# Kernel tuning notes

Measured on AMD Instinct MI355X. Metric: run time of the kernel, lower is better.

The kernel has to match this reference:

```python
import jax, jax.numpy as jnp
import numpy as np

H, DD, NCLS, NELEM, NPROP = 256, 32, 8, 11, 14
B, N = 4, 4096
ENC = NELEM + NPROP  # 25

_DIMS = [("dc1", ENC, H), ("dc21", H, DD), ("dc22", H, DD),
         ("in1", ENC, H), ("in2", H, H), ("in3", H, H),
         ("conv", H, H),
         ("id1", H, H), ("id2", H, H), ("id3", H, H),
         ("oid", H, NCLS), ("och", H, 2),
         ("m1", H + NCLS, H + NCLS), ("m2", H + NCLS, H), ("m3", H, H), ("om", H, 3)]


def setup_inputs() -> dict:
    key = jax.random.key(0)
    ks = jax.random.split(key, 2 + len(_DIMS))
    X = jax.random.normal(ks[0], (B, N, 15), jnp.float32)
    ids = jax.random.randint(ks[1], (B, N), 0, NELEM).astype(jnp.float32)
    X = X.at[:, :, 0].set(ids)
    d = {"X": X}
    for i, (name, di, do) in enumerate(_DIMS):
        W = jax.random.normal(ks[2 + i], (di, do), jnp.float32) / np.sqrt(di)
        d["W_" + name] = W
        d["b_" + name] = jnp.zeros((do,), jnp.float32)
    return d


def reference(X, W_dc1, b_dc1, W_dc21, b_dc21, W_dc22, b_dc22,
              W_in1, b_in1, W_in2, b_in2, W_in3, b_in3,
              W_conv, b_conv,
              W_id1, b_id1, W_id2, b_id2, W_id3, b_id3,
              W_oid, b_oid, W_och, b_och,
              W_m1, b_m1, W_m2, b_m2, W_m3, b_m3, W_om, b_om):
    act = jax.nn.selu
    # input encoding: one-hot element id (stop-grad via int cast) + properties, then selu
    onehot = jax.nn.one_hot(X[:, :, 0].astype(jnp.int32), NELEM, dtype=X.dtype)
    enc = act(jnp.concatenate([onehot, X[:, :, 1:]], axis=-1))  # [B,N,25]
    # distance coordinates
    h = act(enc @ W_dc1 + b_dc1)
    c1 = h @ W_dc21 + b_dc21  # [B,N,DD]
    c2 = h @ W_dc22 + b_dc22
    # pairwise distance -> exp adjacency
    na = jnp.sum(c1 * c1, -1)[:, :, None]
    nb = jnp.sum(c2 * c2, -1)[:, None, :]
    Dsq = jnp.clip(na - 2.0 * jnp.einsum('bnd,bmd->bnm', c1, c2) + nb, 1e-12, 1e12)
    adj = jnp.exp(-jnp.sqrt(Dsq))  # [B,N,N]
    # node MLP
    x = act(enc @ W_in1 + b_in1)
    x = act(x @ W_in2 + b_in2)
    x = act(x @ W_in3 + b_in3)
    # GraphConv: adj^k @ (x W) + b, k=4 (in-degree norm computed but unused upstream)
    x = act(jnp.einsum('bnm,bmh->bnh', adj ** 4, x @ W_conv) + b_conv)
    # id head
    a = act(x @ W_id1 + b_id1)
    a = act(a @ W_id2 + b_id2)
    a = act(a @ W_id3 + b_id3)
    out_id_logits = a @ W_oid + b_oid  # [B,N,8]
    out_charge = a @ W_och + b_och     # [B,N,2]
    # momentum head
    xb = jnp.concatenate([x, act(out_id_logits)], axis=-1)
    bb = act(xb @ W_m1 + b_m1)
    bb = act(bb @ W_m2 + b_m2)
    bb = act(bb @ W_m3 + b_m3)
    corr = bb @ W_om + b_om  # [B,N,3]
    mom = jnp.stack([X[:, :, 2] + corr[:, :, 0],
                     X[:, :, 3] + corr[:, :, 1],
                     X[:, :, 4] + corr[:, :, 2]], axis=-1)
    return jnp.concatenate([out_id_logits, mom, out_charge], axis=-1)  # [B,N,13]
```

## Files before the change

### kernel.cpp

```cpp
#include <hip/hip_runtime.h>
#include <cstddef>
#include <cstdint>

#define MROWS 16384
#define NSEQ  4096
#define ASTR  296
#define SELU_SCALE  1.0507009873554805f
#define SELU_ASCALE 1.7580993408473766f

typedef short bf16x8 __attribute__((ext_vector_type(8)));
typedef float f32x4  __attribute__((ext_vector_type(4)));

__device__ __forceinline__ float selu_f(float x) {
    return x > 0.f ? SELU_SCALE * x : SELU_ASCALE * (__expf(x) - 1.f);
}
__device__ __forceinline__ unsigned short f2bf(float x) {
    union { float f; unsigned int u; } v; v.f = x;
    unsigned int r = v.u + 0x7fffu + ((v.u >> 16) & 1u);
    return (unsigned short)(r >> 16);
}
__device__ __forceinline__ unsigned short t2bf(float x) {
    union { float f; unsigned int u; } v; v.f = x;
    return (unsigned short)(v.u >> 16);
}

struct PrepEnt { const float* W; unsigned short* WT; int N, K, Nfill, ldw, tileOff, tilesK; };
struct PrepArgs {
    PrepEnt e[16];
    const float *b21, *b22, *boid, *boch, *bdc1, *bin1;
    float *bc12, *boo, *bcat;
};
__global__ __launch_bounds__(256) void prep_kernel(PrepArgs pa) {
    if (blockIdx.y == 1) {
        if (blockIdx.x == 0) {
            int t = threadIdx.x;
            if (t < 32) pa.bc12[t] = pa.b21[t];
            else if (t < 64) pa.bc12[t] = pa.b22[t - 32];
            else if (t < 128) {
                int j = t - 64;
                pa.boo[j] = j < 8 ? pa.boid[j] : (j < 10 ? pa.boch[j - 8] : 0.f);
            }
        } else if (blockIdx.x == 1) {
            pa.bcat[threadIdx.x] = pa.bdc1[threadIdx.x];
        } else if (blockIdx.x == 2) {
            pa.bcat[256 + threadIdx.x] = pa.bin1[threadIdx.x];
        }
        return;
    }
    int bx = blockIdx.x;
    int ei = 0;
#pragma unroll
    for (int e = 1; e < 16; ++e)
        if (bx >= pa.e[e].tileOff) ei = e;
    PrepEnt E = pa.e[ei];
    int local = bx - E.tileOff;
    int tn = local / E.tilesK, tk = local - tn * E.tilesK;
    int k0 = tk * 32, n0 = tn * 32;

    __shared__ float ts[32][33];
    int t = threadIdx.x;
    int kl = t >> 3, nl4 = (t & 7) * 4;
    {
        int gk = k0 + kl;
#pragma unroll
        for (int j = 0; j < 4; ++j) {
            int gn = n0 + nl4 + j;
            float v = (gk < E.K && gn < E.N) ? E.W[(size_t)gk * E.N + gn] : 0.f;
            ts[nl4 + j][kl] = v;
        }
    }
    __syncthreads();
    int nl = t >> 3, kl4 = (t & 7) * 4;
    if (n0 + nl < E.Nfill) {
        ushort4 o;
        o.x = f2bf(ts[nl][kl4 + 0]);
        o.y = f2bf(ts[nl][kl4 + 1]);
        o.z = f2bf(ts[nl][kl4 + 2]);
        o.w = f2bf(ts[nl][kl4 + 3]);
        *(ushort4*)(E.WT + (size_t)(n0 + nl) * E.ldw + k0 + kl4) = o;
    }
}

template <int MT, int NT>
__device__ __forceinline__ void zero_acc(f32x4 (&acc)[MT][NT]) {
#pragma unroll
    for (int i = 0; i < MT; ++i)
#pragma unroll
        for (int nt = 0; nt < NT; ++nt) acc[i][nt] = (f32x4){0.f, 0.f, 0.f, 0.f};
}

template <int MT, int NT, int K>
__device__ __forceinline__ void compute_tiles(
    f32x4 (&acc)[MT][NT],
    const unsigned short* __restrict__ src, int sstr,
    const unsigned short* __restrict__ WT, int ldw,
    int col0, int ln)
{
    int quad = ln >> 4, l15 = ln & 15;
    const unsigned short* wbase = WT + (size_t)(col0 + l15) * ldw + quad * 8;
    bf16x8 bcur[NT];
#pragma unroll
    for (int nt = 0; nt < NT; ++nt)
        bcur[nt] = *(const bf16x8*)(wbase + nt * 16 * ldw);
#pragma unroll
    for (int k0 = 0; k0 < K; k0 += 32) {
        bf16x8 bnxt[NT];
        if (k0 + 32 < K) {
#pragma unroll
            for (int nt = 0; nt < NT; ++nt)
                bnxt[nt] = *(const bf16x8*)(wbase + nt * 16 * ldw + k0 + 32);
        }
#pragma unroll
        for (int i = 0; i < MT; ++i) {
            bf16x8 af = *(const bf16x8*)(src + (i * 16 + l15) * sstr + k0 + quad * 8);
#pragma unroll
            for (int nt = 0; nt < NT; ++nt)
                acc[i][nt] = __builtin_amdgcn_mfma_f32_16x16x32_bf16(af, bcur[nt], acc[i][nt], 0, 0, 0);
        }
        if (k0 + 32 < K) {
#pragma unroll
            for (int nt = 0; nt < NT; ++nt) bcur[nt] = bnxt[nt];
        }
    }
}

template <int MT, int NT>
__device__ __forceinline__ void store_tiles(
    f32x4 (&acc)[MT][NT], unsigned short* __restrict__ dst,
    int col0, const float* __restrict__ bias, int Nreal, int act, int ln)
{
    int quad = ln >> 4, l15 = ln & 15;
#pragma unroll
    for (int nt = 0; nt < NT; ++nt) {
        int col = col0 + nt * 16 + l15;
        float bv = (bias && col < Nreal) ? bias[col] : 0.f;
#pragma unroll
        for (int i = 0; i < MT; ++i) {
#pragma unroll
            for (int r = 0; r < 4; ++r) {
                int row = i * 16 + quad * 4 + r;
                float v = acc[i][nt][r] + bv;
                if (act) v = selu_f(v);
                if (col >= Nreal) v = 0.f;
                dst[row * ASTR + col] = f2bf(v);
            }
        }
    }
}

__global__ __launch_bounds__(512) void pre_mega(
    const float* __restrict__ X,
    const unsigned short* __restrict__ WTd, const float* __restrict__ bcat,
    const unsigned short* __restrict__ WTc12, const float* __restrict__ bc12,
    const unsigned short* __restrict__ WTin2, const float* __restrict__ b_in2,
    const unsigned short* __restrict__ WTin3, const float* __restrict__ b_in3,
    const unsigned short* __restrict__ WTconv,
    unsigned short* __restrict__ c1b, unsigned short* __restrict__ c2b,
    float* __restrict__ n1, float* __restrict__ n2,
    unsigned short* __restrict__ xwTb)
{
    __shared__ unsigned short encs[64 * 32];
    __shared__ unsigned short bufA[64 * ASTR];
    __shared__ unsigned short bufB[64 * ASTR];
    __shared__ float c12s[64 * 68];

    int tid = threadIdx.x, wv = tid >> 6, ln = tid & 63;
    int quad = ln >> 4, l15 = ln & 15;
    int row0 = blockIdx.x * 64;

#pragma unroll
    for (int p = 0; p < 4; ++p) {
        int idx = p * 512 + tid;
        int row = idx >> 5, col = idx & 31;
        float v = 0.f;
        if (col < 11) {
            int id = (int)X[(size_t)(row0 + row) * 15];
            v = (id == col) ? SELU_SCALE : 0.f;
        } else if (col < 25) {
            v = selu_f(X[(size_t)(row0 + row) * 15 + 1 + (col - 11)]);
        }
        encs[row * 32 + col] = f2bf(v);
    }
    __syncthreads();

#pragma unroll
    for (int ph = 0; ph < 2; ++ph) {
        f32x4 acc[4][2]; zero_acc<4, 2>(acc);
        compute_tiles<4, 2, 32>(acc, encs, 32, WTd + (size_t)ph * 256 * 32, 32, wv * 32, ln);
        store_tiles<4, 2>(acc, ph ? bufB : bufA, wv * 32, bcat + ph * 256, 256, 1, ln);
    }
    __syncthreads();

    if (wv < 2) {
        f32x4 acc[4][2]; zero_acc<4, 2>(acc);
        compute_tiles<4, 2, 256>(acc, bufA, ASTR, WTc12, 256, wv * 32, ln);
#pragma unroll
        for (int nt = 0; nt < 2; ++nt) {
            int col = wv * 32 + nt * 16 + l15;
            float bv = bc12[col];
#pragma unroll
            for (int i = 0; i < 4; ++i)
#pragma unroll
                for (int r = 0; r < 4; ++r)
                    c12s[(i * 16 + quad * 4 + r) * 68 + col] = acc[i][nt][r] + bv;
        }
    }
    __syncthreads();

    if (tid < 64) {
        int grow = row0 + tid;
        const float* p = &c12s[tid * 68];
        float s1 = 0.f, s2 = 0.f;
        unsigned int o1[16], o2[16];
#pragma unroll
        for (int k = 0; k < 32; k += 2) {
            float a0 = p[k], a1 = p[k + 1];
            s1 += a0 * a0 + a1 * a1;
            o1[k >> 1] = (unsigned)f2bf(a0) | ((unsigned)f2bf(a1) << 16);
            float b0 = p[32 + k], b1 = p[33 + k];
            s2 += b0 * b0 + b1 * b1;
            o2[k >> 1] = (unsigned)f2bf(b0) | ((unsigned)f2bf(b1) << 16);
        }
        uint4* d1 = (uint4*)(c1b + (size_t)grow * 32);
        uint4* d2 = (uint4*)(c2b + (size_t)grow * 32);
#pragma unroll
        for (int j = 0; j < 4; ++j) {
            d1[j] = make_uint4(o1[4 * j], o1[4 * j + 1], o1[4 * j + 2], o1[4 * j + 3]);
            d2[j] = make_uint4(o2[4 * j], o2[4 * j + 1], o2[4 * j + 2], o2[4 * j + 3]);
        }
        n1[grow] = s1;
        n2[grow] = s2;
    }

    {
        f32x4 acc[4][2]; zero_acc<4, 2>(acc);
        compute_tiles<4, 2, 256>(acc, bufB, ASTR, WTin2, 256, wv * 32, ln);
        store_tiles<4, 2>(acc, bufA, wv * 32, b_in2, 256, 1, ln);
    }
    __syncthreads();
    {
        f32x4 acc[4][2]; zero_acc<4, 2>(acc);
        compute_tiles<4, 2, 256>(acc, bufA, ASTR, WTin3, 256, wv * 32, ln);
        store_tiles<4, 2>(acc, bufB, wv * 32, b_in3, 256, 1, ln);
    }
    __syncthreads();
    {
        f32x4 acc[4][2]; zero_acc<4, 2>(acc);
        compute_tiles<4, 2, 256>(acc, bufB, ASTR, WTconv, 256, wv * 32, ln);
        store_tiles<4, 2>(acc, bufA, wv * 32, nullptr, 256, 0, ln);
    }
    __syncthreads();

    int b = row0 >> 12;
    int c0 = (row0 & 4095) >> 5;
#pragma unroll
    for (int p = 0; p < 4; ++p) {
        int idx = p * 512 + tid;
        int h = idx >> 3, mg = idx & 7;
        unsigned int w[4];
#pragma unroll
        for (int j = 0; j < 4; ++j) {
            unsigned int lo = bufA[(mg * 8 + 2 * j) * ASTR + h];
            unsigned int hi = bufA[(mg * 8 + 2 * j + 1) * ASTR + h];
            w[j] = lo | (hi << 16);
        }
        *(uint4*)(xwTb + ((size_t)((b * 128 + c0 + (mg >> 2)) * 256 + h) * 32) + (mg & 3) * 8) =
            make_uint4(w[0], w[1], w[2], w[3]);
    }
}

__global__ __launch_bounds__(512, 4) void adj_conv_mfma(
    const unsigned short* __restrict__ c1b, const unsigned short* __restrict__ c2b,
    const float* __restrict__ n1, const float* __restrict__ n2,
    const unsigned short* __restrict__ xwTb, const float* __restrict__ bconv,
    unsigned short* __restrict__ xc)
{
    __shared__ unsigned short wls[2][32][72];

    int tid = threadIdx.x, wv = tid >> 6, ln = tid & 63, quad = ln >> 4, l15 = ln & 15;
    int blk = blockIdx.x;
    int b = (blk >> 1) & 3;
    int iidx = ((blk >> 3) << 1) | (blk & 1);
    int i0 = iidx * 32;
    size_t base = (size_t)b * NSEQ;

    int it = wv & 1;
    int mt = wv >> 1;

    bf16x8 c1f = *(const bf16x8*)(c1b + (base + i0 + it * 16 + l15) * 32 + quad * 8);
    float4 n1v = *(const float4*)(n1 + base + i0 + it * 16 + quad * 4);
    const unsigned short* xwb = xwTb + (size_t)b * 128 * 256 * 32;

    f32x4 acc[2][2];
#pragma unroll
    for (int i = 0; i < 2; ++i)
#pragma unroll
        for (int j = 0; j < 2; ++j) acc[i][j] = (f32x4){0.f, 0.f, 0.f, 0.f};

    bf16x8 c2f = *(const bf16x8*)(c2b + (base + mt * 16 + l15) * 32 + quad * 8);
    float nn2 = n2[base + mt * 16 + l15];
    bf16x8 bfc[2][2];
#pragma unroll
    for (int ht = 0; ht < 2; ++ht)
#pragma unroll
        for (int ks = 0; ks < 2; ++ks)
            bfc[ht][ks] = *(const bf16x8*)(xwb +
                ((size_t)ks * 256 + wv * 32 + ht * 16 + l15) * 32 + quad * 8);

#pragma unroll 2
    for (int itr = 0; itr < 64; ++itr) {
        int p = itr & 1;
        {
            f32x4 dotv = (f32x4){0.f, 0.f, 0.f, 0.f};
            dotv = __builtin_amdgcn_mfma_f32_16x16x32_bf16(c1f, c2f, dotv, 0, 0, 0);
#pragma unroll
            for (int r = 0; r < 4; ++r) {
                float D = fmaf(-2.f, dotv[r], n1v[r] + nn2);
                float t = __builtin_amdgcn_sqrtf(fmaxf(D, 1e-12f));
                wls[p][it * 16 + quad * 4 + r][mt * 16 + l15] = t2bf(__expf(t * -4.f));
            }
        }
        __syncthreads();

        bf16x8 af[2][2];
#pragma unroll
        for (int mi = 0; mi < 2; ++mi)
#pragma unroll
            for (int ks = 0; ks < 2; ++ks)
                af[mi][ks] = *(const bf16x8*)&wls[p][mi * 16 + l15][ks * 32 + quad * 8];

        bf16x8 bfn[2][2];
        if (itr < 63) {
            int m0n = (itr + 1) * 64;
            c2f = *(const bf16x8*)(c2b + (base + m0n + mt * 16 + l15) * 32 + quad * 8);
            nn2 = n2[base + m0n + mt * 16 + l15];
#pragma unroll
            for (int ht = 0; ht < 2; ++ht)
#pragma unroll
                for (int ks = 0; ks < 2; ++ks)
                    bfn[ht][ks] = *(const bf16x8*)(xwb +
                        ((size_t)((itr + 1) * 2 + ks) * 256 + wv * 32 + ht * 16 + l15) * 32 + quad * 8);
        }

#pragma unroll
        for (int mi = 0; mi < 2; ++mi)
#pragma unroll
            for (int ht = 0; ht < 2; ++ht)
#pragma unroll
                for (int ks = 0; ks < 2; ++ks)
                    acc[mi][ht] = __builtin_amdgcn_mfma_f32_16x16x32_bf16(
                        af[mi][ks], bfc[ht][ks], acc[mi][ht], 0, 0, 0);
        if (itr < 63) {
#pragma unroll
            for (int ht = 0; ht < 2; ++ht)
#pragma unroll
                for (int ks = 0; ks < 2; ++ks)
                    bfc[ht][ks] = bfn[ht][ks];
        }
    }

#pragma unroll
    for (int mi = 0; mi < 2; ++mi) {
#pragma unroll
        for (int ht = 0; ht < 2; ++ht) {
            int h = wv * 32 + ht * 16 + l15;
            float bv = bconv[h];
#pragma unroll
            for (int r = 0; r < 4; ++r) {
                int irow = i0 + mi * 16 + quad * 4 + r;
                xc[(base + irow) * 256 + h] = f2bf(selu_f(acc[mi][ht][r] + bv));
            }
        }
    }
}

__global__ __launch_bounds__(512) void post_mega(
    const float* __restrict__ X, const unsigned short* __restrict__ xc,
    const unsigned short* __restrict__ WTid1, const float* __restrict__ b_id1,
    const unsigned short* __restrict__ WTid2, const float* __restrict__ b_id2,
    const unsigned short* __restrict__ WTid3, const float* __restrict__ b_id3,
    const unsigned short* __restrict__ WToo, const float* __restrict__ boo,
    const unsigned short* __restrict__ WTm1, const float* __restrict__ b_m1,
    const unsigned short* __restrict__ WTm2, const float* __restrict__ b_m2,
    const unsigned short* __restrict__ WTm3, const float* __restrict__ b_m3,
    const unsigned short* __restrict__ WTom, const float* __restrict__ b_om,
    float* __restrict__ out)
{
    __shared__ unsigned short xcs[64 * ASTR];
    __shared__ unsigned short bufA[64 * ASTR];
    __shared__ unsigned short bufB[64 * ASTR];
    __shared__ float lgs[64 * 16];

    int tid = threadIdx.x, wv = tid >> 6, ln = tid & 63;
    int quad = ln >> 4, l15 = ln & 15;
    int row0 = blockIdx.x * 64;

#pragma unroll
    for (int p = 0; p < 4; ++p) {
        int idx = p * 512 + tid;
        int row = idx >> 5, c8 = (idx & 31) * 8;
        *(uint4*)&xcs[row * ASTR + c8] = *(const uint4*)(xc + (size_t)(row0 + row) * 256 + c8);
    }
#pragma unroll
    for (int p = 0; p < 5; ++p) {
        int idx = p * 512 + tid;
        int row = idx / 40, c = 256 + idx - row * 40;
        xcs[row * ASTR + c] = 0;
        bufB[row * ASTR + c] = 0;
    }
    __syncthreads();

    {
        f32x4 acc[4][2]; zero_acc<4, 2>(acc);
        compute_tiles<4, 2, 256>(acc, xcs, ASTR, WTid1, 256, wv * 32, ln);
        store_tiles<4, 2>(acc, bufA, wv * 32, b_id1, 256, 1, ln);
    }
    __syncthreads();
    {
        f32x4 acc[4][2]; zero_acc<4, 2>(acc);
        compute_tiles<4, 2, 256>(acc, bufA, ASTR, WTid2, 256, wv * 32, ln);
        store_tiles<4, 2>(acc, bufB, wv * 32, b_id2, 256, 1, ln);
    }
    __syncthreads();
    {
        f32x4 acc[4][2]; zero_acc<4, 2>(acc);
        compute_tiles<4, 2, 256>(acc, bufB, ASTR, WTid3, 256, wv * 32, ln);
        store_tiles<4, 2>(acc, bufA, wv * 32, b_id3, 256, 1, ln);
    }
    __syncthreads();
    if (wv == 0) {
        f32x4 acc[4][1]; zero_acc<4, 1>(acc);
        compute_tiles<4, 1, 256>(acc, bufA, ASTR, WToo, 256, 0, ln);
        float bv = boo[l15];
#pragma unroll
        for (int i = 0; i < 4; ++i)
#pragma unroll
            for (int r = 0; r < 4; ++r)
                lgs[(i * 16 + quad * 4 + r) * 16 + l15] = acc[i][0][r] + bv;
    }
    __syncthreads();
    if (tid < 64) {
        float* op = out + (size_t)(row0 + tid) * 13;
#pragma unroll
        for (int c = 0; c < 8; ++c) {
            float lg = lgs[tid * 16 + c];
            op[c] = lg;
            xcs[tid * ASTR + 256 + c] = f2bf(selu_f(lg));
        }
        op[11] = lgs[tid * 16 + 8];
        op[12] = lgs[tid * 16 + 9];
    }
    __syncthreads();
    {
        f32x4 acc[4][2]; zero_acc<4, 2>(acc);
        compute_tiles<4, 2, 288>(acc, xcs, ASTR, WTm1, 288, wv * 32, ln);
        store_tiles<4, 2>(acc, bufB, wv * 32, b_m1, 264, 1, ln);
        if (wv == 0) {
            f32x4 acx[4][1]; zero_acc<4, 1>(acx);
            compute_tiles<4, 1, 288>(acx, xcs, ASTR, WTm1, 288, 256, ln);
            store_tiles<4, 1>(acx, bufB, 256, b_m1, 264, 1, ln);
        }
    }
    __syncthreads();
    {
        f32x4 acc[4][2]; zero_acc<4, 2>(acc);
        compute_tiles<4, 2, 288>(acc, bufB, ASTR, WTm2, 288, wv * 32, ln);
        store_tiles<4, 2>(acc, bufA, wv * 32, b_m2, 256, 1, ln);
    }
    __syncthreads();
    {
        f32x4 acc[4][2]; zero_acc<4, 2>(acc);
        compute_tiles<4, 2, 256>(acc, bufA, ASTR, WTm3, 256, wv * 32, ln);
        store_tiles<4, 2>(acc, bufB, wv * 32, b_m3, 256, 1, ln);
    }
    __syncthreads();
    if (wv == 0) {
        f32x4 acc[4][1]; zero_acc<4, 1>(acc);
        compute_tiles<4, 1, 256>(acc, bufB, ASTR, WTom, 256, 0, ln);
        if (l15 < 3) {
            float bv = b_om[l15];
#pragma unroll
            for (int i = 0; i < 4; ++i)
#pragma unroll
                for (int r = 0; r < 4; ++r) {
                    int grow = row0 + i * 16 + quad * 4 + r;
                    out[(size_t)grow * 13 + 8 + l15] =
                        X[(size_t)grow * 15 + 2 + l15] + acc[i][0][r] + bv;
                }
        }
    }
}

extern "C" void kernel_launch(void* const* d_in, const int* in_sizes, int n_in,
                              void* d_out, int out_size, void* d_ws, size_t ws_size,
                              hipStream_t stream) {
    (void)in_sizes; (void)n_in; (void)out_size; (void)ws_size;

    const float* X = (const float*)d_in[0];
    const float* W_dc1 = (const float*)d_in[1];  const float* b_dc1 = (const float*)d_in[2];
    const float* W_dc21 = (const float*)d_in[3]; const float* b_dc21 = (const float*)d_in[4];
    const float* W_dc22 = (const float*)d_in[5]; const float* b_dc22 = (const float*)d_in[6];
    const float* W_in1 = (const float*)d_in[7];  const float* b_in1 = (const float*)d_in[8];
    const float* W_in2 = (const float*)d_in[9];  const float* b_in2 = (const float*)d_in[10];
    const float* W_in3 = (const float*)d_in[11]; const float* b_in3 = (const float*)d_in[12];
    const float* W_conv = (const float*)d_in[13]; const float* b_conv = (const float*)d_in[14];
    const float* W_id1 = (const float*)d_in[15]; const float* b_id1 = (const float*)d_in[16];
    const float* W_id2 = (const float*)d_in[17]; const float* b_id2 = (const float*)d_in[18];
    const float* W_id3 = (const float*)d_in[19]; const float* b_id3 = (const float*)d_in[20];
    const float* W_oid = (const float*)d_in[21]; const float* b_oid = (const float*)d_in[22];
    const float* W_och = (const float*)d_in[23]; const float* b_och = (const float*)d_in[24];
    const float* W_m1 = (const float*)d_in[25];  const float* b_m1 = (const float*)d_in[26];
    const float* W_m2 = (const float*)d_in[27];  const float* b_m2 = (const float*)d_in[28];
    const float* W_m3 = (const float*)d_in[29];  const float* b_m3 = (const float*)d_in[30];
    const float* W_om = (const float*)d_in[31];  const float* b_om = (const float*)d_in[32];

    const size_t M = MROWS;
    char* pw = (char*)d_ws;
    auto alloc = [&](size_t bytes) -> void* {
        void* r = (void*)pw;
        pw += (bytes + 255) & ~(size_t)255;
        return r;
    };
    unsigned short* c1b = (unsigned short*)alloc(M * 32 * 2);
    unsigned short* c2b = (unsigned short*)alloc(M * 32 * 2);
    float* n1 = (float*)alloc(M * 4);
    float* n2 = (float*)alloc(M * 4);
    unsigned short* xwTb = (unsigned short*)alloc((size_t)4 * 128 * 256 * 32 * 2);
    unsigned short* xcb = (unsigned short*)alloc(M * 256 * 2);
    unsigned short* WTd = (unsigned short*)alloc(512 * 32 * 2);
    unsigned short* WTc12 = (unsigned short*)alloc(64 * 256 * 2);
    unsigned short* WTin2 = (unsigned short*)alloc(256 * 256 * 2);
    unsigned short* WTin3 = (unsigned short*)alloc(256 * 256 * 2);
    unsigned short* WTconv = (unsigned short*)alloc(256 * 256 * 2);
    unsigned short* WTid1 = (unsigned short*)alloc(256 * 256 * 2);
    unsigned short* WTid2 = (unsigned short*)alloc(256 * 256 * 2);
    unsigned short* WTid3 = (unsigned short*)alloc(256 * 256 * 2);
    unsigned short* WTm3 = (unsigned short*)alloc(256 * 256 * 2);
    unsigned short* WToo = (unsigned short*)alloc(64 * 256 * 2);
    unsigned short* WTm1 = (unsigned short*)alloc(320 * 288 * 2);
    unsigned short* WTm2 = (unsigned short*)alloc(256 * 288 * 2);
    unsigned short* WTom = (unsigned short*)alloc(64 * 256 * 2);
    float* bc12 = (float*)alloc(64 * 4);
    float* boo = (float*)alloc(64 * 4);
    float* bcat = (float*)alloc(512 * 4);

    PrepArgs pa;
    int off = 0;
    auto ent = [&](const float* W, unsigned short* WT, int N, int K, int Nf, int ldw) {
        PrepEnt e; e.W = W; e.WT = WT; e.N = N; e.K = K; e.Nfill = Nf; e.ldw = ldw;
        e.tileOff = off; e.tilesK = ldw / 32;
        off += ((Nf + 31) / 32) * e.tilesK;
        return e;
    };
    pa.e[0]  = ent(W_dc1,  WTd,              256, 25,  256, 32);
    pa.e[1]  = ent(W_in1,  WTd + 256 * 32,   256, 25,  256, 32);
    pa.e[2]  = ent(W_dc21, WTc12,            32,  256, 32,  256);
    pa.e[3]  = ent(W_dc22, WTc12 + 32 * 256, 32,  256, 32,  256);
    pa.e[4]  = ent(W_in2,  WTin2,            256, 256, 256, 256);
    pa.e[5]  = ent(W_in3,  WTin3,            256, 256, 256, 256);
    pa.e[6]  = ent(W_conv, WTconv,           256, 256, 256, 256);
    pa.e[7]  = ent(W_id1,  WTid1,            256, 256, 256, 256);
    pa.e[8]  = ent(W_id2,  WTid2,            256, 256, 256, 256);
    pa.e[9]  = ent(W_id3,  WTid3,            256, 256, 256, 256);
    pa.e[10] = ent(W_m3,   WTm3,             256, 256, 256, 256);
    pa.e[11] = ent(W_oid,  WToo,             8,   256, 8,   256);
    pa.e[12] = ent(W_och,  WToo + 8 * 256,   2,   256, 56,  256);
    pa.e[13] = ent(W_m1,   WTm1,             264, 264, 320, 288);
    pa.e[14] = ent(W_m2,   WTm2,             256, 264, 256, 288);
    pa.e[15] = ent(W_om,   WTom,             3,   256, 64,  256);
    pa.b21 = b_dc21; pa.b22 = b_dc22; pa.boid = b_oid; pa.boch = b_och;
    pa.bdc1 = b_dc1; pa.bin1 = b_in1;
    pa.bc12 = bc12; pa.boo = boo; pa.bcat = bcat;
    prep_kernel<<<dim3(off, 2), 256, 0, stream>>>(pa);

    pre_mega<<<dim3(256), 512, 0, stream>>>(X, WTd, bcat, WTc12, bc12,
                                            WTin2, b_in2, WTin3, b_in3, WTconv,
                                            c1b, c2b, n1, n2, xwTb);

    adj_conv_mfma<<<dim3(512), 512, 0, stream>>>(c1b, c2b, n1, n2, xwTb, b_conv, xcb);

    post_mega<<<dim3(256), 512, 0, stream>>>(X, xcb,
                                             WTid1, b_id1, WTid2, b_id2, WTid3, b_id3,
                                             WToo, boo, WTm1, b_m1, WTm2, b_m2,
                                             WTm3, b_m3, WTom, b_om, (float*)d_out);
}
```

Before: 269.0 us.

## Pre-swizzle weights into MFMA fragment order and deepen B-operand prefetch

```diff
diff --git a/kernel.cpp b/kernel.cpp
--- a/kernel.cpp
+++ b/kernel.cpp
@@ -24,7 +24,7 @@
     return (unsigned short)(v.u >> 16);
 }
 
-struct PrepEnt { const float* W; unsigned short* WT; int N, K, Nfill, ldw, tileOff, tilesK; };
+struct PrepEnt { const float* W; unsigned short* WTf; int N, K, ntiles, KS, tileOff, tilesN; };
 struct PrepArgs {
     PrepEnt e[16];
     const float *b21, *b22, *boid, *boch, *bdc1, *bin1;
@@ -36,9 +36,9 @@
             int t = threadIdx.x;
             if (t < 32) pa.bc12[t] = pa.b21[t];
             else if (t < 64) pa.bc12[t] = pa.b22[t - 32];
-            else if (t < 128) {
+            else if (t < 96) {
                 int j = t - 64;
-                pa.boo[j] = j < 8 ? pa.boid[j] : (j < 10 ? pa.boch[j - 8] : 0.f);
+                pa.boo[j] = j < 8 ? pa.boid[j] : ((j >= 16 && j < 18) ? pa.boch[j - 16] : 0.f);
             }
         } else if (blockIdx.x == 1) {
             pa.bcat[threadIdx.x] = pa.bdc1[threadIdx.x];
@@ -54,13 +54,13 @@
         if (bx >= pa.e[e].tileOff) ei = e;
     PrepEnt E = pa.e[ei];
     int local = bx - E.tileOff;
-    int tn = local / E.tilesK, tk = local - tn * E.tilesK;
+    int tn = local / E.KS, tk = local - tn * E.KS;
     int k0 = tk * 32, n0 = tn * 32;
 
     __shared__ float ts[32][33];
     int t = threadIdx.x;
-    int kl = t >> 3, nl4 = (t & 7) * 4;
-    {
+    {
+        int kl = t >> 3, nl4 = (t & 7) * 4;
         int gk = k0 + kl;
 #pragma unroll
         for (int j = 0; j < 4; ++j) {
@@ -71,13 +71,16 @@
     }
     __syncthreads();
     int nl = t >> 3, kl4 = (t & 7) * 4;
-    if (n0 + nl < E.Nfill) {
+    int n = n0 + nl;
+    if (n < E.ntiles * 16) {
         ushort4 o;
         o.x = f2bf(ts[nl][kl4 + 0]);
         o.y = f2bf(ts[nl][kl4 + 1]);
         o.z = f2bf(ts[nl][kl4 + 2]);
         o.w = f2bf(ts[nl][kl4 + 3]);
-        *(ushort4*)(E.WT + (size_t)(n0 + nl) * E.ldw + k0 + kl4) = o;
+        size_t dst = ((size_t)(n >> 4) * E.KS + tk) * 512 +
+                     (size_t)((kl4 >> 3) * 16 + (n & 15)) * 8 + (kl4 & 7);
+        *(ushort4*)(E.WTf + dst) = o;
     }
 }
 
@@ -93,33 +96,43 @@
 __device__ __forceinline__ void compute_tiles(
     f32x4 (&acc)[MT][NT],
     const unsigned short* __restrict__ src, int sstr,
-    const unsigned short* __restrict__ WT, int ldw,
+    const unsigned short* __restrict__ WTf,
     int col0, int ln)
 {
+    constexpr int KS = (K + 31) / 32;
     int quad = ln >> 4, l15 = ln & 15;
-    const unsigned short* wbase = WT + (size_t)(col0 + l15) * ldw + quad * 8;
-    bf16x8 bcur[NT];
+    const unsigned short* wp = WTf + (size_t)(col0 >> 4) * (KS * 512) + ln * 8;
+    bf16x8 bc[NT], bn[NT];
 #pragma unroll
     for (int nt = 0; nt < NT; ++nt)
-        bcur[nt] = *(const bf16x8*)(wbase + nt * 16 * ldw);
-#pragma unroll
-    for (int k0 = 0; k0 < K; k0 += 32) {
-        bf16x8 bnxt[NT];
-        if (k0 + 32 < K) {
+        bc[nt] = *(const bf16x8*)(wp + nt * (KS * 512));
+    if (KS > 1) {
+#pragma unroll
+        for (int nt = 0; nt < NT; ++nt)
+            bn[nt] = *(const bf16x8*)(wp + nt * (KS * 512) + 512);
+    }
+#pragma unroll
+    for (int ks = 0; ks < KS; ++ks) {
+        bf16x8 b2[NT];
+        if (ks + 2 < KS) {
 #pragma unroll
             for (int nt = 0; nt < NT; ++nt)
-                bnxt[nt] = *(const bf16x8*)(wbase + nt * 16 * ldw + k0 + 32);
+                b2[nt] = *(const bf16x8*)(wp + nt * (KS * 512) + (ks + 2) * 512);
         }
 #pragma unroll
         for (int i = 0; i < MT; ++i) {
-            bf16x8 af = *(const bf16x8*)(src + (i * 16 + l15) * sstr + k0 + quad * 8);
+            bf16x8 af = *(const bf16x8*)(src + (i * 16 + l15) * sstr + ks * 32 + quad * 8);
 #pragma unroll
             for (int nt = 0; nt < NT; ++nt)
-                acc[i][nt] = __builtin_amdgcn_mfma_f32_16x16x32_bf16(af, bcur[nt], acc[i][nt], 0, 0, 0);
-        }
-        if (k0 + 32 < K) {
-#pragma unroll
-            for (int nt = 0; nt < NT; ++nt) bcur[nt] = bnxt[nt];
+                acc[i][nt] = __builtin_amdgcn_mfma_f32_16x16x32_bf16(af, bc[nt], acc[i][nt], 0, 0, 0);
+        }
+        if (ks + 1 < KS) {
+#pragma unroll
+            for (int nt = 0; nt < NT; ++nt) bc[nt] = bn[nt];
+        }
+        if (ks + 2 < KS) {
+#pragma unroll
+            for (int nt = 0; nt < NT; ++nt) bn[nt] = b2[nt];
         }
     }
 }
@@ -150,11 +163,11 @@
 
 __global__ __launch_bounds__(512) void pre_mega(
     const float* __restrict__ X,
-    const unsigned short* __restrict__ WTd, const float* __restrict__ bcat,
-    const unsigned short* __restrict__ WTc12, const float* __restrict__ bc12,
-    const unsigned short* __restrict__ WTin2, const float* __restrict__ b_in2,
-    const unsigned short* __restrict__ WTin3, const float* __restrict__ b_in3,
-    const unsigned short* __restrict__ WTconv,
+    const unsigned short* __restrict__ WTdF, const float* __restrict__ bcat,
+    const unsigned short* __restrict__ WTc12F, const float* __restrict__ bc12,
+    const unsigned short* __restrict__ WTin2F, const float* __restrict__ b_in2,
+    const unsigned short* __restrict__ WTin3F, const float* __restrict__ b_in3,
+    const unsigned short* __restrict__ WTconvF,
     unsigned short* __restrict__ c1b, unsigned short* __restrict__ c2b,
     float* __restrict__ n1, float* __restrict__ n2,
     unsigned short* __restrict__ xwTb)
@@ -186,14 +199,14 @@
 #pragma unroll
     for (int ph = 0; ph < 2; ++ph) {
         f32x4 acc[4][2]; zero_acc<4, 2>(acc);
-        compute_tiles<4, 2, 32>(acc, encs, 32, WTd + (size_t)ph * 256 * 32, 32, wv * 32, ln);
+        compute_tiles<4, 2, 32>(acc, encs, 32, WTdF + (size_t)ph * 16 * 512, wv * 32, ln);
         store_tiles<4, 2>(acc, ph ? bufB : bufA, wv * 32, bcat + ph * 256, 256, 1, ln);
     }
     __syncthreads();
 
     if (wv < 2) {
         f32x4 acc[4][2]; zero_acc<4, 2>(acc);
-        compute_tiles<4, 2, 256>(acc, bufA, ASTR, WTc12, 256, wv * 32, ln);
+        compute_tiles<4, 2, 256>(acc, bufA, ASTR, WTc12F, wv * 32, ln);
 #pragma unroll
         for (int nt = 0; nt < 2; ++nt) {
             int col = wv * 32 + nt * 16 + l15;
@@ -234,19 +247,19 @@
 
     {
         f32x4 acc[4][2]; zero_acc<4, 2>(acc);
-        compute_tiles<4, 2, 256>(acc, bufB, ASTR, WTin2, 256, wv * 32, ln);
+        compute_tiles<4, 2, 256>(acc, bufB, ASTR, WTin2F, wv * 32, ln);
         store_tiles<4, 2>(acc, bufA, wv * 32, b_in2, 256, 1, ln);
     }
     __syncthreads();
     {
         f32x4 acc[4][2]; zero_acc<4, 2>(acc);
-        compute_tiles<4, 2, 256>(acc, bufA, ASTR, WTin3, 256, wv * 32, ln);
+        compute_tiles<4, 2, 256>(acc, bufA, ASTR, WTin3F, wv * 32, ln);
         store_tiles<4, 2>(acc, bufB, wv * 32, b_in3, 256, 1, ln);
     }
     __syncthreads();
     {
         f32x4 acc[4][2]; zero_acc<4, 2>(acc);
-        compute_tiles<4, 2, 256>(acc, bufB, ASTR, WTconv, 256, wv * 32, ln);
+        compute_tiles<4, 2, 256>(acc, bufB, ASTR, WTconvF, wv * 32, ln);
         store_tiles<4, 2>(acc, bufA, wv * 32, nullptr, 256, 0, ln);
     }
     __syncthreads();
@@ -289,7 +302,12 @@
 
     bf16x8 c1f = *(const bf16x8*)(c1b + (base + i0 + it * 16 + l15) * 32 + quad * 8);
     float4 n1v = *(const float4*)(n1 + base + i0 + it * 16 + quad * 4);
-    const unsigned short* xwb = xwTb + (size_t)b * 128 * 256 * 32;
+
+    const unsigned short* xwp0 = xwTb + (size_t)b * (128 * 256 * 32)
+                               + ((size_t)(wv * 32 + l15) * 32 + quad * 8);
+    const unsigned short* xwp1 = xwp0 + 8192;
+    const unsigned short* c2p  = c2b + (base + mt * 16 + l15) * 32 + quad * 8;
+    const float* n2p = n2 + base + mt * 16 + l15;
 
     f32x4 acc[2][2];
 #pragma unroll
@@ -297,15 +315,15 @@
 #pragma unroll
         for (int j = 0; j < 2; ++j) acc[i][j] = (f32x4){0.f, 0.f, 0.f, 0.f};
 
-    bf16x8 c2f = *(const bf16x8*)(c2b + (base + mt * 16 + l15) * 32 + quad * 8);
-    float nn2 = n2[base + mt * 16 + l15];
+    bf16x8 c2f = *(const bf16x8*)c2p;
+    float nn2 = *n2p;
     bf16x8 bfc[2][2];
 #pragma unroll
-    for (int ht = 0; ht < 2; ++ht)
-#pragma unroll
-        for (int ks = 0; ks < 2; ++ks)
-            bfc[ht][ks] = *(const bf16x8*)(xwb +
-                ((size_t)ks * 256 + wv * 32 + ht * 16 + l15) * 32 + quad * 8);
+    for (int ht = 0; ht < 2; ++ht) {
+        bfc[ht][0] = *(const bf16x8*)(xwp0 + ht * 512);
+        bfc[ht][1] = *(const bf16x8*)(xwp1 + ht * 512);
+    }
+    xwp0 += 16384; xwp1 += 16384; c2p += 2048; n2p += 64;
 
 #pragma unroll 2
     for (int itr = 0; itr < 64; ++itr) {
@@ -331,15 +349,14 @@
 
         bf16x8 bfn[2][2];
         if (itr < 63) {
-            int m0n = (itr + 1) * 64;
-            c2f = *(const bf16x8*)(c2b + (base + m0n + mt * 16 + l15) * 32 + quad * 8);
-            nn2 = n2[base + m0n + mt * 16 + l15];
-#pragma unroll
-            for (int ht = 0; ht < 2; ++ht)
-#pragma unroll
-                for (int ks = 0; ks < 2; ++ks)
-                    bfn[ht][ks] = *(const bf16x8*)(xwb +
-                        ((size_t)((itr + 1) * 2 + ks) * 256 + wv * 32 + ht * 16 + l15) * 32 + quad * 8);
+            c2f = *(const bf16x8*)c2p;
+            nn2 = *n2p;
+#pragma unroll
+            for (int ht = 0; ht < 2; ++ht) {
+                bfn[ht][0] = *(const bf16x8*)(xwp0 + ht * 512);
+                bfn[ht][1] = *(const bf16x8*)(xwp1 + ht * 512);
+            }
+            xwp0 += 16384; xwp1 += 16384; c2p += 2048; n2p += 64;
         }
 
 #pragma unroll
@@ -376,20 +393,20 @@
 
 __global__ __launch_bounds__(512) void post_mega(
     const float* __restrict__ X, const unsigned short* __restrict__ xc,
-    const unsigned short* __restrict__ WTid1, const float* __restrict__ b_id1,
-    const unsigned short* __restrict__ WTid2, const float* __restrict__ b_id2,
-    const unsigned short* __restrict__ WTid3, const float* __restrict__ b_id3,
-    const unsigned short* __restrict__ WToo, const float* __restrict__ boo,
-    const unsigned short* __restrict__ WTm1, const float* __restrict__ b_m1,
-    const unsigned short* __restrict__ WTm2, const float* __restrict__ b_m2,
-    const unsigned short* __restrict__ WTm3, const float* __restrict__ b_m3,
-    const unsigned short* __restrict__ WTom, const float* __restrict__ b_om,
+    const unsigned short* __restrict__ WTid1F, const float* __restrict__ b_id1,
+    const unsigned short* __restrict__ WTid2F, const float* __restrict__ b_id2,
+    const unsigned short* __restrict__ WTid3F, const float* __restrict__ b_id3,
+    const unsigned short* __restrict__ WTooF, const float* __restrict__ boo,
+    const unsigned short* __restrict__ WTm1F, const float* __restrict__ b_m1,
+    const unsigned short* __restrict__ WTm2F, const float* __restrict__ b_m2,
+    const unsigned short* __restrict__ WTm3F, const float* __restrict__ b_m3,
+    const unsigned short* __restrict__ WTomF, const float* __restrict__ b_om,
     float* __restrict__ out)
 {
     __shared__ unsigned short xcs[64 * ASTR];
     __shared__ unsigned short bufA[64 * ASTR];
     __shared__ unsigned short bufB[64 * ASTR];
-    __shared__ float lgs[64 * 16];
+    __shared__ float lgs[64 * 32];
 
     int tid = threadIdx.x, wv = tid >> 6, ln = tid & 63;
     int quad = ln >> 4, l15 = ln & 15;
@@ -412,71 +429,75 @@
 
     {
         f32x4 acc[4][2]; zero_acc<4, 2>(acc);
-        compute_tiles<4, 2, 256>(acc, xcs, ASTR, WTid1, 256, wv * 32, ln);
+        compute_tiles<4, 2, 256>(acc, xcs, ASTR, WTid1F, wv * 32, ln);
         store_tiles<4, 2>(acc, bufA, wv * 32, b_id1, 256, 1, ln);
     }
     __syncthreads();
     {
         f32x4 acc[4][2]; zero_acc<4, 2>(acc);
-        compute_tiles<4, 2, 256>(acc, bufA, ASTR, WTid2, 256, wv * 32, ln);
+        compute_tiles<4, 2, 256>(acc, bufA, ASTR, WTid2F, wv * 32, ln);
         store_tiles<4, 2>(acc, bufB, wv * 32, b_id2, 256, 1, ln);
     }
     __syncthreads();
     {
         f32x4 acc[4][2]; zero_acc<4, 2>(acc);
-        compute_tiles<4, 2, 256>(acc, bufB, ASTR, WTid3, 256, wv * 32, ln);
+        compute_tiles<4, 2, 256>(acc, bufB, ASTR, WTid3F, wv * 32, ln);
         store_tiles<4, 2>(acc, bufA, wv * 32, b_id3, 256, 1, ln);
     }
     __syncthreads();
     if (wv == 0) {
-        f32x4 acc[4][1]; zero_acc<4, 1>(acc);
-        compute_tiles<4, 1, 256>(acc, bufA, ASTR, WToo, 256, 0, ln);
-        float bv = boo[l15];
-#pragma unroll
-        for (int i = 0; i < 4; ++i)
-#pragma unroll
-            for (int r = 0; r < 4; ++r)
-                lgs[(i * 16 + quad * 4 + r) * 16 + l15] = acc[i][0][r] + bv;
+        f32x4 acc[4][2]; zero_acc<4, 2>(acc);
+        compute_tiles<4, 2, 256>(acc, bufA, ASTR, WTooF, 0, ln);
+#pragma unroll
+        for (int nt = 0; nt < 2; ++nt) {
+            int col = nt * 16 + l15;
+            float bv = boo[col];
+#pragma unroll
+            for (int i = 0; i < 4; ++i)
+#pragma unroll
+                for (int r = 0; r < 4; ++r)
+                    lgs[(i * 16 + quad * 4 + r) * 32 + col] = acc[i][nt][r] + bv;
+        }
     }
     __syncthreads();
     if (tid < 64) {
         float* op = out + (size_t)(row0 + tid) * 13;
 #pragma unroll
         for (int c = 0; c < 8; ++c) {
-            float lg = lgs[tid * 16 + c];
+            float lg = lgs[tid * 32 + c];
             op[c] = lg;
             xcs[tid * ASTR + 256 + c] = f2bf(selu_f(lg));
         }
-        op[11] = lgs[tid * 16 + 8];
-        op[12] = lgs[tid * 16 + 9];
-    }
-    __syncthreads();
-    {
-        f32x4 acc[4][2]; zero_acc<4, 2>(acc);
-        compute_tiles<4, 2, 288>(acc, xcs, ASTR, WTm1, 288, wv * 32, ln);
+        op[11] = lgs[tid * 32 + 16];
+        op[12] = lgs[tid * 32 + 17];
+    }
+    __syncthreads();
+    {
+        f32x4 acc[4][2]; zero_acc<4, 2>(acc);
+        compute_tiles<4, 2, 288>(acc, xcs, ASTR, WTm1F, wv * 32, ln);
         store_tiles<4, 2>(acc, bufB, wv * 32, b_m1, 264, 1, ln);
         if (wv == 0) {
             f32x4 acx[4][1]; zero_acc<4, 1>(acx);
-            compute_tiles<4, 1, 288>(acx, xcs, ASTR, WTm1, 288, 256, ln);
+            compute_tiles<4, 1, 288>(acx, xcs, ASTR, WTm1F, 256, ln);
             store_tiles<4, 1>(acx, bufB, 256, b_m1, 264, 1, ln);
         }
     }
     __syncthreads();
     {
         f32x4 acc[4][2]; zero_acc<4, 2>(acc);
-        compute_tiles<4, 2, 288>(acc, bufB, ASTR, WTm2, 288, wv * 32, ln);
+        compute_tiles<4, 2, 288>(acc, bufB, ASTR, WTm2F, wv * 32, ln);
         store_tiles<4, 2>(acc, bufA, wv * 32, b_m2, 256, 1, ln);
     }
     __syncthreads();
     {
         f32x4 acc[4][2]; zero_acc<4, 2>(acc);
-        compute_tiles<4, 2, 256>(acc, bufA, ASTR, WTm3, 256, wv * 32, ln);
+        compute_tiles<4, 2, 256>(acc, bufA, ASTR, WTm3F, wv * 32, ln);
         store_tiles<4, 2>(acc, bufB, wv * 32, b_m3, 256, 1, ln);
     }
     __syncthreads();
     if (wv == 0) {
         f32x4 acc[4][1]; zero_acc<4, 1>(acc);
-        compute_tiles<4, 1, 256>(acc, bufB, ASTR, WTom, 256, 0, ln);
+        compute_tiles<4, 1, 256>(acc, bufB, ASTR, WTomF, 0, ln);
         if (l15 < 3) {
             float bv = b_om[l15];
 #pragma unroll
@@ -527,60 +548,62 @@
     float* n2 = (float*)alloc(M * 4);
     unsigned short* xwTb = (unsigned short*)alloc((size_t)4 * 128 * 256 * 32 * 2);
     unsigned short* xcb = (unsigned short*)alloc(M * 256 * 2);
-    unsigned short* WTd = (unsigned short*)alloc(512 * 32 * 2);
-    unsigned short* WTc12 = (unsigned short*)alloc(64 * 256 * 2);
-    unsigned short* WTin2 = (unsigned short*)alloc(256 * 256 * 2);
-    unsigned short* WTin3 = (unsigned short*)alloc(256 * 256 * 2);
-    unsigned short* WTconv = (unsigned short*)alloc(256 * 256 * 2);
-    unsigned short* WTid1 = (unsigned short*)alloc(256 * 256 * 2);
-    unsigned short* WTid2 = (unsigned short*)alloc(256 * 256 * 2);
-    unsigned short* WTid3 = (unsigned short*)alloc(256 * 256 * 2);
-    unsigned short* WTm3 = (unsigned short*)alloc(256 * 256 * 2);
-    unsigned short* WToo = (unsigned short*)alloc(64 * 256 * 2);
-    unsigned short* WTm1 = (unsigned short*)alloc(320 * 288 * 2);
-    unsigned short* WTm2 = (unsigned short*)alloc(256 * 288 * 2);
-    unsigned short* WTom = (unsigned short*)alloc(64 * 256 * 2);
+    unsigned short* WTdF   = (unsigned short*)alloc((size_t)2 * 16 * 1 * 512 * 2);
+    unsigned short* WTc12F = (unsigned short*)alloc((size_t)4 * 8 * 512 * 2);
+    unsigned short* WTin2F = (unsigned short*)alloc((size_t)16 * 8 * 512 * 2);
+    unsigned short* WTin3F = (unsigned short*)alloc((size_t)16 * 8 * 512 * 2);
+    unsigned short* WTconvF = (unsigned short*)alloc((size_t)16 * 8 * 512 * 2);
+    unsigned short* WTid1F = (unsigned short*)alloc((size_t)16 * 8 * 512 * 2);
+    unsigned short* WTid2F = (unsigned short*)alloc((size_t)16 * 8 * 512 * 2);
+    unsigned short* WTid3F = (unsigned short*)alloc((size_t)16 * 8 * 512 * 2);
+    unsigned short* WTm3F  = (unsigned short*)alloc((size_t)16 * 8 * 512 * 2);
+    unsigned short* WTooF  = (unsigned short*)alloc((size_t)2 * 8 * 512 * 2);
+    unsigned short* WTm1F  = (unsigned short*)alloc((size_t)17 * 9 * 512 * 2);
+    unsigned short* WTm2F  = (unsigned short*)alloc((size_t)16 * 9 * 512 * 2);
+    unsigned short* WTomF  = (unsigned short*)alloc((size_t)1 * 8 * 512 * 2);
     float* bc12 = (float*)alloc(64 * 4);
-    float* boo = (float*)alloc(64 * 4);
+    float* boo = (float*)alloc(32 * 4);
     float* bcat = (float*)alloc(512 * 4);
 
     PrepArgs pa;
     int off = 0;
-    auto ent = [&](const float* W, unsigned short* WT, int N, int K, int Nf, int ldw) {
-        PrepEnt e; e.W = W; e.WT = WT; e.N = N; e.K = K; e.Nfill = Nf; e.ldw = ldw;
-        e.tileOff = off; e.tilesK = ldw / 32;
-        off += ((Nf + 31) / 32) * e.tilesK;
+    auto ent = [&](const float* W, unsigned short* WTf, int N, int K, int ntiles) {
+        PrepEnt e; e.W = W; e.WTf = WTf; e.N = N; e.K = K; e.ntiles = ntiles;
+        e.KS = (K + 31) / 32;
+        e.tilesN = (ntiles * 16 + 31) / 32;
+        e.tileOff = off;
+        off += e.tilesN * e.KS;
         return e;
     };
-    pa.e[0]  = ent(W_dc1,  WTd,              256, 25,  256, 32);
-    pa.e[1]  = ent(W_in1,  WTd + 256 * 32,   256, 25,  256, 32);
-    pa.e[2]  = ent(W_dc21, WTc12,            32,  256, 32,  256);
-    pa.e[3]  = ent(W_dc22, WTc12 + 32 * 256, 32,  256, 32,  256);
-    pa.e[4]  = ent(W_in2,  WTin2,            256, 256, 256, 256);
-    pa.e[5]  = ent(W_in3,  WTin3,            256, 256, 256, 256);
-    pa.e[6]  = ent(W_conv, WTconv,           256, 256, 256, 256);
-    pa.e[7]  = ent(W_id1,  WTid1,            256, 256, 256, 256);
-    pa.e[8]  = ent(W_id2,  WTid2,            256, 256, 256, 256);
-    pa.e[9]  = ent(W_id3,  WTid3,            256, 256, 256, 256);
-    pa.e[10] = ent(W_m3,   WTm3,             256, 256, 256, 256);
-    pa.e[11] = ent(W_oid,  WToo,             8,   256, 8,   256);
-    pa.e[12] = ent(W_och,  WToo + 8 * 256,   2,   256, 56,  256);
-    pa.e[13] = ent(W_m1,   WTm1,             264, 264, 320, 288);
-    pa.e[14] = ent(W_m2,   WTm2,             256, 264, 256, 288);
-    pa.e[15] = ent(W_om,   WTom,             3,   256, 64,  256);
+    pa.e[0]  = ent(W_dc1,  WTdF,                256, 25,  16);
+    pa.e[1]  = ent(W_in1,  WTdF + 16 * 512,     256, 25,  16);
+    pa.e[2]  = ent(W_dc21, WTc12F,              32,  256, 2);
+    pa.e[3]  = ent(W_dc22, WTc12F + 2 * 8 * 512, 32, 256, 2);
+    pa.e[4]  = ent(W_in2,  WTin2F,              256, 256, 16);
+    pa.e[5]  = ent(W_in3,  WTin3F,              256, 256, 16);
+    pa.e[6]  = ent(W_conv, WTconvF,             256, 256, 16);
+    pa.e[7]  = ent(W_id1,  WTid1F,              256, 256, 16);
+    pa.e[8]  = ent(W_id2,  WTid2F,              256, 256, 16);
+    pa.e[9]  = ent(W_id3,  WTid3F,              256, 256, 16);
+    pa.e[10] = ent(W_m3,   WTm3F,               256, 256, 16);
+    pa.e[11] = ent(W_oid,  WTooF,               8,   256, 1);
+    pa.e[12] = ent(W_och,  WTooF + 8 * 512,     2,   256, 1);
+    pa.e[13] = ent(W_m1,   WTm1F,               264, 264, 17);
+    pa.e[14] = ent(W_m2,   WTm2F,               256, 264, 16);
+    pa.e[15] = ent(W_om,   WTomF,               3,   256, 1);
     pa.b21 = b_dc21; pa.b22 = b_dc22; pa.boid = b_oid; pa.boch = b_och;
     pa.bdc1 = b_dc1; pa.bin1 = b_in1;
     pa.bc12 = bc12; pa.boo = boo; pa.bcat = bcat;
     prep_kernel<<<dim3(off, 2), 256, 0, stream>>>(pa);
 
-    pre_mega<<<dim3(256), 512, 0, stream>>>(X, WTd, bcat, WTc12, bc12,
-                                            WTin2, b_in2, WTin3, b_in3, WTconv,
+    pre_mega<<<dim3(256), 512, 0, stream>>>(X, WTdF, bcat, WTc12F, bc12,
+                                            WTin2F, b_in2, WTin3F, b_in3, WTconvF,
                                             c1b, c2b, n1, n2, xwTb);
 
     adj_conv_mfma<<<dim3(512), 512, 0, stream>>>(c1b, c2b, n1, n2, xwTb, b_conv, xcb);
 
     post_mega<<<dim3(256), 512, 0, stream>>>(X, xcb,
-                                             WTid1, b_id1, WTid2, b_id2, WTid3, b_id3,
-                                             WToo, boo, WTm1, b_m1, WTm2, b_m2,
-                                             WTm3, b_m3, WTom, b_om, (float*)d_out);
-}
+                                             WTid1F, b_id1, WTid2F, b_id2, WTid3F, b_id3,
+                                             WTooF, boo, WTm1F, b_m1, WTm2F, b_m2,
+                                             WTm3F, b_m3, WTomF, b_om, (float*)d_out);
+}
```

Result: faster. 261.9 us (-2.6%).
